# Optimization experiments

Measured on AMD Instinct MI355X. Metric: run time of the kernel, lower is better.

The kernel has to match this reference:

```python
import jax, jax.numpy as jnp
import numpy as np

NUM_HEADS = 16
HEAD_DIM = 64
HIDDEN = NUM_HEADS * HEAD_DIM  # 1024
MAX_POS = 1024


def setup_inputs() -> dict:
    key = jax.random.key(0)
    ks = jax.random.split(key, 6)
    B, L, H = 8, 1024, HIDDEN
    hidden_states = jax.random.normal(ks[0], (B, L, H), dtype=jnp.float32)
    attention_mask = jnp.zeros((B, 1, 1, L), dtype=jnp.float32)
    scale = 0.02  # keep pre-softmax logits in a sane range
    Wq = jax.random.normal(ks[1], (H, H), dtype=jnp.float32) * scale
    Wk = jax.random.normal(ks[2], (H, H), dtype=jnp.float32) * scale
    Wv = jax.random.normal(ks[3], (H, H), dtype=jnp.float32) * scale
    bq = jnp.zeros((H,), dtype=jnp.float32)
    bk = jnp.zeros((H,), dtype=jnp.float32)
    bv = jnp.zeros((H,), dtype=jnp.float32)
    dist_emb = jax.random.normal(ks[4], (2 * MAX_POS - 1, HEAD_DIM), dtype=jnp.float32) * scale
    return {"hidden_states": hidden_states, "attention_mask": attention_mask,
            "Wq": Wq, "bq": bq, "Wk": Wk, "bk": bk, "Wv": Wv, "bv": bv,
            "dist_emb": dist_emb}


def _split_heads(x):
    # [B, L, H] -> [B, nH, L, hd]
    B, L, _ = x.shape
    return x.reshape(B, L, NUM_HEADS, HEAD_DIM).transpose(0, 2, 1, 3)


def reference(hidden_states, attention_mask, Wq, bq, Wk, bk, Wv, bv, dist_emb):
    B, L, H = hidden_states.shape
    q = _split_heads(hidden_states @ Wq.T + bq)  # [B,h,L,d]
    k = _split_heads(hidden_states @ Wk.T + bk)
    v = _split_heads(hidden_states @ Wv.T + bv)

    scores = jnp.einsum("bhld,bhrd->bhlr", q, k)

    # relative_key_query positional bias
    pos_l = jnp.arange(L)[:, None]
    pos_r = jnp.arange(L)[None, :]
    dist_idx = pos_l - pos_r + MAX_POS - 1          # [L, L], in [0, 2*MAX_POS-2]
    pos_emb = dist_emb[dist_idx]                    # [L, L, d]
    scores = scores + jnp.einsum("bhld,lrd->bhlr", q, pos_emb)
    scores = scores + jnp.einsum("bhrd,lrd->bhlr", k, pos_emb)

    scores = scores / jnp.sqrt(jnp.float32(HEAD_DIM))
    scores = scores + attention_mask                # additive mask broadcast [B,1,1,L]
    probs = jax.nn.softmax(scores, axis=-1)         # dropout = identity (eval)
    ctx = jnp.einsum("bhlr,bhrd->bhld", probs, v)
    ctx = ctx.transpose(0, 2, 1, 3).reshape(B, L, H)
    return ctx
```

## Files before the change

kernel.cpp:

```cpp
#include <hip/hip_runtime.h>
#include <stdint.h>

typedef short s16x8 __attribute__((ext_vector_type(8)));
typedef float f32x4 __attribute__((ext_vector_type(4)));

#define MFMA16(a, b, c) __builtin_amdgcn_mfma_f32_16x16x32_bf16((a), (b), (c), 0, 0, 0)

__device__ __forceinline__ ushort f2b(float f) {
  union { float f; uint32_t u; } x; x.f = f;
  uint32_t r = x.u + 0x7fffu + ((x.u >> 16) & 1u);
  return (ushort)(r >> 16);
}
__device__ __forceinline__ float b2f(ushort s) {
  union { uint32_t u; float f; } x; x.u = ((uint32_t)s) << 16;
  return x.f;
}
__device__ __forceinline__ uint32_t pack2t(float a, float b) {
  return __builtin_amdgcn_perm(__float_as_uint(b), __float_as_uint(a), 0x07060302u);
}

__global__ __launch_bounds__(256) void cast_f32_bf16(const float* __restrict__ src,
                                                     ushort* __restrict__ dst, int n) {
  int i = (blockIdx.x * 256 + threadIdx.x) * 4;
  if (i + 4 <= n) {
    float4 v = *(const float4*)(src + i);
    ushort4 o; o.x = f2b(v.x); o.y = f2b(v.y); o.z = f2b(v.z); o.w = f2b(v.w);
    *(ushort4*)(dst + i) = o;
  }
}

__device__ __forceinline__ void gload16(const void* g, void* l) {
  __builtin_amdgcn_global_load_lds((const __attribute__((address_space(1))) void*)g,
                                   (__attribute__((address_space(3))) void*)l, 16, 0, 0);
}

__global__ __launch_bounds__(256) void qkv_gemm(
    const ushort* __restrict__ hb, const ushort* __restrict__ wb,
    const float* __restrict__ bq, const float* __restrict__ bk, const float* __restrict__ bv,
    ushort* __restrict__ qb, ushort* __restrict__ kb, ushort* __restrict__ vt) {
  __shared__ ushort As[128 * 32];
  __shared__ ushort Bs[128 * 32];
  const int tid = threadIdx.x;
  const int w = tid >> 6, lane = tid & 63, quad = lane >> 4, l16 = lane & 15;
  const int m0 = blockIdx.y * 128, n0 = blockIdx.x * 128;

  const int srow = w * 32 + (lane >> 2);
  const int scol = (lane & 3) * 8;
  const ushort* ga = hb + (size_t)(m0 + srow) * 1024 + scol;
  const ushort* gw = wb + (size_t)(n0 + srow) * 1024 + scol;
  ushort* lA0 = As + (w * 32) * 32;
  ushort* lA1 = As + (w * 32 + 16) * 32;
  ushort* lB0 = Bs + (w * 32) * 32;
  ushort* lB1 = Bs + (w * 32 + 16) * 32;

  f32x4 acc[4][4];
#pragma unroll
  for (int mt = 0; mt < 4; ++mt)
#pragma unroll
    for (int nt = 0; nt < 4; ++nt) acc[mt][nt] = (f32x4){0.f, 0.f, 0.f, 0.f};

  const int wm = (w >> 1) * 64, wn = (w & 1) * 64;

  for (int k0 = 0; k0 < 1024; k0 += 32) {
    gload16(ga + k0, lA0);
    gload16(ga + k0 + 16 * 1024, lA1);
    gload16(gw + k0, lB0);
    gload16(gw + k0 + 16 * 1024, lB1);
    __syncthreads();
    s16x8 af[4], bfr[4];
#pragma unroll
    for (int mt = 0; mt < 4; ++mt)
      af[mt] = *(const s16x8*)(As + (wm + 16 * mt + l16) * 32 + quad * 8);
#pragma unroll
    for (int nt = 0; nt < 4; ++nt)
      bfr[nt] = *(const s16x8*)(Bs + (wn + 16 * nt + l16) * 32 + quad * 8);
#pragma unroll
    for (int mt = 0; mt < 4; ++mt)
#pragma unroll
      for (int nt = 0; nt < 4; ++nt)
        acc[mt][nt] = MFMA16(af[mt], bfr[nt], acc[mt][nt]);
    __syncthreads();
  }

  const int mat = n0 >> 10;
  const float* bias = (mat == 0) ? bq : ((mat == 1) ? bk : bv);
  const int b = m0 >> 10;
#pragma unroll
  for (int mt = 0; mt < 4; ++mt) {
    int mbase = m0 + wm + 16 * mt + 4 * quad;
#pragma unroll
    for (int nt = 0; nt < 4; ++nt) {
      int n = n0 + wn + 16 * nt + l16;
      int o = n & 1023; int hh = o >> 6; int d = o & 63;
      float bsv = bias[o];
#pragma unroll
      for (int reg = 0; reg < 4; ++reg) {
        int l = (mbase + reg) & 1023;
        ushort bx = f2b(acc[mt][nt][reg] + bsv);
        if (mat == 0)      qb[(((size_t)(b * 16 + hh)) * 1024 + l) * 64 + d] = bx;
        else if (mat == 1) kb[(((size_t)(b * 16 + hh)) * 1024 + l) * 64 + d] = bx;
        else               vt[(((size_t)(b * 16 + hh)) * 64 + d) * 1024 + l] = bx;
      }
    }
  }
}

#define KR  0
#define VR  8192
#define ER  16384
#define SER 28672
#define PR  35072

__device__ __forceinline__ const s16x8* fragp(const ushort* base, int row, int cb) {
  return (const s16x8*)(base + row * 64 + ((cb ^ (row & 7)) * 8));
}

__global__ __launch_bounds__(256, 2) void attn_kernel(
    const ushort* __restrict__ qb, const ushort* __restrict__ kb,
    const ushort* __restrict__ vt, const ushort* __restrict__ eb,
    const float* __restrict__ mask, float* __restrict__ out) {
  __shared__ __align__(16) ushort sm[39168];
  const int tid = threadIdx.x;
  const int w = tid >> 6, lane = tid & 63, quad = lane >> 4, l16 = lane & 15;
  const int bh = blockIdx.y, b = bh >> 4, h = bh & 15;
  const int l0 = blockIdx.x * 64;

  const int srow = lane >> 3;
  const int colb = ((lane & 7) ^ srow) * 8;
  const int row0 = w * 8 + srow;

  const ushort* kp = kb + ((size_t)bh * 1024 + row0) * 64 + colb;
  const ushort* vp = vt + ((size_t)bh * 64 + row0) * 1024 + colb;
  const float* maskp = mask + b * 1024 + l16;

  const int p0 = blockIdx.x % 3;

  {
    const ushort* qp = qb + ((size_t)bh * 1024 + l0 + row0) * 64 + colb;
    gload16(qp,         sm + PR + w * 512);
    gload16(qp + 2048,  sm + PR + 2048 + w * 512);
    gload16(kp,         sm + KR + w * 512);
    gload16(kp + 2048,  sm + KR + 2048 + w * 512);
    gload16(vp,         sm + VR + w * 512);
    gload16(vp + 32768, sm + VR + 2048 + w * 512);
    const int t0i = l0 + 960;
#pragma unroll
    for (int c2 = 0; c2 < 4; ++c2) {
      int jb = w * 8 + 32 * c2;
      int seg = p0 + (jb >> 6); if (seg >= 3) seg -= 3;
      int t = t0i + jb + srow; if (t > 2046) t = 2046;
      gload16(eb + (size_t)t * 64 + colb, sm + ER + seg * 4096 + (jb & 63) * 64);
    }
  }
  __syncthreads();

  s16x8 aq0, aq1;
  {
    int r = w * 16 + l16;
    aq0 = *fragp(sm + PR, r, quad);
    aq1 = *fragp(sm + PR, r, quad + 4);
  }

  float rsum[4];
  f32x4 o_acc[4];
#pragma unroll
  for (int r = 0; r < 4; ++r) rsum[r] = 0.f;
#pragma unroll
  for (int nt = 0; nt < 4; ++nt) o_acc[nt] = (f32x4){0.f, 0.f, 0.f, 0.f};

  const float LOG2E = 1.44269504088896f;
  const float SC = 0.125f * LOG2E;

  int s0 = p0;

  for (int it = 0; it < 16; ++it) {
    const int p = it & 1;
    const int r0 = it * 64;
    if (it > 0) __syncthreads();

    {
      const int rn = (r0 + 64) & 1023;
      gload16(kp + rn * 64,        sm + KR + 4096 * (1 - p) + w * 512);
      gload16(kp + rn * 64 + 2048, sm + KR + 4096 * (1 - p) + 2048 + w * 512);
      gload16(vp + rn,             sm + VR + 4096 * (1 - p) + w * 512);
      gload16(vp + rn + 32768,     sm + VR + 4096 * (1 - p) + 2048 + w * 512);
      int pnew = s0 + 2; if (pnew >= 3) pnew -= 3;
      const int tb = l0 + 960 - r0 - 64;
#pragma unroll
      for (int c2 = 0; c2 < 2; ++c2) {
        int o = w * 8 + 32 * c2;
        int t = tb + o + srow; t = t < 0 ? 0 : (t > 2046 ? 2046 : t);
        gload16(eb + (size_t)t * 64 + colb, sm + ER + pnew * 4096 + o * 64);
      }
    }
    float mkv[4];
#pragma unroll
    for (int nt = 0; nt < 4; ++nt) mkv[nt] = maskp[r0 + 16 * nt] * LOG2E;

    const ushort* Kb = sm + KR + 4096 * p;
    const int sA = s0; int sB = s0 + 1; if (sB >= 3) sB -= 3;

    f32x4 zv[4];
#pragma unroll
    for (int nt = 0; nt < 4; ++nt) {
      int r = 16 * nt + l16;
      s16x8 bk0 = *fragp(Kb, r, quad);
      s16x8 bk1 = *fragp(Kb, r, quad + 4);
      f32x4 z = (f32x4){0.f, 0.f, 0.f, 0.f};
      z = MFMA16(aq0, bk0, z);
      z = MFMA16(aq1, bk1, z);
      zv[nt] = z;
    }
    s16x8 ak0, ak1;
    {
      int r = w * 16 + l16;
      ak0 = *fragp(Kb, r, quad);
      ak1 = *fragp(Kb, r, quad + 4);
    }

    f32x4 d1[5];
#pragma unroll
    for (int i = 0; i < 5; ++i) {
      int blk = w + i;
      int seg = (blk & 4) ? sB : sA;
      int row = seg * 64 + (blk & 3) * 16 + l16;
      s16x8 be0 = *fragp(sm + ER, row, quad);
      s16x8 be1 = *fragp(sm + ER, row, quad + 4);
      f32x4 z = (f32x4){0.f, 0.f, 0.f, 0.f};
      z = MFMA16(aq0, be0, z);
      z = MFMA16(aq1, be1, z);
      d1[i] = z;
    }
#pragma unroll
    for (int r = 0; r < 4; ++r) {
      int idx = (quad * 16 + ((4 * quad + r + 15 - l16) & 15)) * 4;
      float bp[5];
#pragma unroll
      for (int i = 0; i < 5; ++i)
        bp[i] = __int_as_float(__builtin_amdgcn_ds_bpermute(idx, __float_as_int(d1[i][r])));
      bool cnd = (4 * quad + r) > l16;
#pragma unroll
      for (int nt = 0; nt < 4; ++nt)
        zv[nt][r] += cnd ? bp[4 - nt] : bp[3 - nt];
    }

#pragma unroll
    for (int i = 0; i < 5; ++i) {
      int blk = 3 - w + i;
      int seg = (blk & 4) ? sB : sA;
      int row = seg * 64 + (blk & 3) * 16 + l16;
      s16x8 be0 = *fragp(sm + ER, row, quad);
      s16x8 be1 = *fragp(sm + ER, row, quad + 4);
      f32x4 z = (f32x4){0.f, 0.f, 0.f, 0.f};
      z = MFMA16(ak0, be0, z);
      z = MFMA16(ak1, be1, z);
      uint2 pk; pk.x = pack2t(z[0], z[1]); pk.y = pack2t(z[2], z[3]);
      *(uint2*)(sm + SER + w * 1600 + (16 * i + l16) * 20 + 4 * quad) = pk;
    }
    __syncthreads();

    const int bb = (w * 16 + 4 * quad + 15 - l16) * 20 + l16;
#pragma unroll
    for (int nt = 0; nt < 4; ++nt) {
#pragma unroll
      for (int reg = 0; reg < 4; ++reg) {
        float z2 = (zv[nt][reg] + b2f(sm[SER + bb + nt * 1600 + reg * 20])) * SC + mkv[nt];
        float pe = exp2f(z2);
        zv[nt][reg] = pe;
        rsum[reg] += pe;
      }
    }

#pragma unroll
    for (int nt = 0; nt < 4; ++nt) {
      int r = 16 * nt + l16;
      int rcb = r >> 3, rlo = r & 7;
#pragma unroll
      for (int reg = 0; reg < 4; ++reg) {
        int l = w * 16 + 4 * quad + reg;
        sm[PR + l * 64 + ((rcb ^ (l & 7)) * 8) + rlo] = f2b(zv[nt][reg]);
      }
    }
    __syncthreads();

    const ushort* Vb = sm + VR + 4096 * p;
#pragma unroll
    for (int kk = 0; kk < 2; ++kk) {
      s16x8 ap = *fragp(sm + PR, w * 16 + l16, kk * 4 + quad);
#pragma unroll
      for (int nt = 0; nt < 4; ++nt) {
        s16x8 bvf = *fragp(Vb, 16 * nt + l16, kk * 4 + quad);
        o_acc[nt] = MFMA16(ap, bvf, o_acc[nt]);
      }
    }

    s0 = (s0 == 0) ? 2 : s0 - 1;
  }

#pragma unroll
  for (int off = 1; off < 16; off <<= 1)
#pragma unroll
    for (int reg = 0; reg < 4; ++reg)
      rsum[reg] += __shfl_xor(rsum[reg], off);

#pragma unroll
  for (int nt = 0; nt < 4; ++nt)
#pragma unroll
    for (int reg = 0; reg < 4; ++reg) {
      int l = l0 + w * 16 + 4 * quad + reg;
      int d = 16 * nt + l16;
      out[((size_t)(b * 1024 + l)) * 1024 + h * 64 + d] = o_acc[nt][reg] / rsum[reg];
    }
}

extern "C" void kernel_launch(void* const* d_in, const int* in_sizes, int n_in,
                              void* d_out, int out_size, void* d_ws, size_t ws_size,
                              hipStream_t stream) {
  const float* hidden = (const float*)d_in[0];
  const float* mask   = (const float*)d_in[1];
  const float* Wq     = (const float*)d_in[2];
  const float* bq     = (const float*)d_in[3];
  const float* Wk     = (const float*)d_in[4];
  const float* bk     = (const float*)d_in[5];
  const float* Wv     = (const float*)d_in[6];
  const float* bv     = (const float*)d_in[7];
  const float* dist   = (const float*)d_in[8];
  float* out = (float*)d_out;

  ushort* ws = (ushort*)d_ws;
  ushort* qb = ws;
  ushort* kb = ws + 8388608;
  ushort* vt = ws + 16777216;
  ushort* hb = ws + 25165824;
  ushort* wb = ws + 33554432;
  ushort* eb = ws + 36700160;

  cast_f32_bf16<<<8192, 256, 0, stream>>>(hidden, hb, 8388608);
  cast_f32_bf16<<<1024, 256, 0, stream>>>(Wq, wb, 1048576);
  cast_f32_bf16<<<1024, 256, 0, stream>>>(Wk, wb + 1048576, 1048576);
  cast_f32_bf16<<<1024, 256, 0, stream>>>(Wv, wb + 2097152, 1048576);
  cast_f32_bf16<<<128, 256, 0, stream>>>(dist, eb, 131008);

  qkv_gemm<<<dim3(24, 64), 256, 0, stream>>>(hb, wb, bq, bk, bv, qb, kb, vt);
  attn_kernel<<<dim3(16, 128), 256, 0, stream>>>(qb, kb, vt, eb, mask, out);
}
```

Measured before the change: 387.2 us.

## Load K/V MFMA fragments directly from global memory and raise attention occupancy

The attention kernel no longer stages K and V tiles through double-buffered LDS. Each lane now loads its K and V MFMA operand fragments straight from global memory (relying on L2 reuse across blocks), which cuts LDS from about 78KB to 45KB and lets launch bounds request 3 blocks per CU. The QKV projection epilogue also writes the transposed V with packed 4-element stores instead of scalar ones. In exchange, K/V global loads are issued within the same iteration they are consumed, with no software prefetch, so load latency may be exposed. Each K row is also fetched redundantly by all four waves.

```diff
diff --git a/kernel.cpp b/kernel.cpp
--- a/kernel.cpp
+++ b/kernel.cpp
@@ -88,38 +88,42 @@
 #pragma unroll
   for (int mt = 0; mt < 4; ++mt) {
     int mbase = m0 + wm + 16 * mt + 4 * quad;
+    int lb = mbase & 1023;
 #pragma unroll
     for (int nt = 0; nt < 4; ++nt) {
       int n = n0 + wn + 16 * nt + l16;
       int o = n & 1023; int hh = o >> 6; int d = o & 63;
       float bsv = bias[o];
-#pragma unroll
-      for (int reg = 0; reg < 4; ++reg) {
-        int l = (mbase + reg) & 1023;
-        ushort bx = f2b(acc[mt][nt][reg] + bsv);
-        if (mat == 0)      qb[(((size_t)(b * 16 + hh)) * 1024 + l) * 64 + d] = bx;
-        else if (mat == 1) kb[(((size_t)(b * 16 + hh)) * 1024 + l) * 64 + d] = bx;
-        else               vt[(((size_t)(b * 16 + hh)) * 64 + d) * 1024 + l] = bx;
-      }
-    }
-  }
-}
-
-#define KR  0
-#define VR  8192
-#define ER  16384
-#define SER 28672
-#define PR  35072
+      if (mat == 2) {
+        ushort4 pk;
+        pk.x = f2b(acc[mt][nt][0] + bsv);
+        pk.y = f2b(acc[mt][nt][1] + bsv);
+        pk.z = f2b(acc[mt][nt][2] + bsv);
+        pk.w = f2b(acc[mt][nt][3] + bsv);
+        *(ushort4*)(vt + (((size_t)(b * 16 + hh)) * 64 + d) * 1024 + lb) = pk;
+      } else {
+        ushort* dst = (mat == 0) ? qb : kb;
+#pragma unroll
+        for (int reg = 0; reg < 4; ++reg)
+          dst[(((size_t)(b * 16 + hh)) * 1024 + lb + reg) * 64 + d] = f2b(acc[mt][nt][reg] + bsv);
+      }
+    }
+  }
+}
+
+#define ER  0
+#define SER 12288
+#define PR  18688
 
 __device__ __forceinline__ const s16x8* fragp(const ushort* base, int row, int cb) {
   return (const s16x8*)(base + row * 64 + ((cb ^ (row & 7)) * 8));
 }
 
-__global__ __launch_bounds__(256, 2) void attn_kernel(
+__global__ __launch_bounds__(256, 3) void attn_kernel(
     const ushort* __restrict__ qb, const ushort* __restrict__ kb,
     const ushort* __restrict__ vt, const ushort* __restrict__ eb,
     const float* __restrict__ mask, float* __restrict__ out) {
-  __shared__ __align__(16) ushort sm[39168];
+  __shared__ __align__(16) ushort sm[22784];
   const int tid = threadIdx.x;
   const int w = tid >> 6, lane = tid & 63, quad = lane >> 4, l16 = lane & 15;
   const int bh = blockIdx.y, b = bh >> 4, h = bh & 15;
@@ -129,8 +133,8 @@
   const int colb = ((lane & 7) ^ srow) * 8;
   const int row0 = w * 8 + srow;
 
-  const ushort* kp = kb + ((size_t)bh * 1024 + row0) * 64 + colb;
-  const ushort* vp = vt + ((size_t)bh * 64 + row0) * 1024 + colb;
+  const ushort* kgl = kb + (size_t)bh * 65536 + l16 * 64 + quad * 8;
+  const ushort* vgl = vt + (size_t)bh * 65536 + l16 * 1024 + quad * 8;
   const float* maskp = mask + b * 1024 + l16;
 
   const int p0 = blockIdx.x % 3;
@@ -139,10 +143,6 @@
     const ushort* qp = qb + ((size_t)bh * 1024 + l0 + row0) * 64 + colb;
     gload16(qp,         sm + PR + w * 512);
     gload16(qp + 2048,  sm + PR + 2048 + w * 512);
-    gload16(kp,         sm + KR + w * 512);
-    gload16(kp + 2048,  sm + KR + 2048 + w * 512);
-    gload16(vp,         sm + VR + w * 512);
-    gload16(vp + 32768, sm + VR + 2048 + w * 512);
     const int t0i = l0 + 960;
 #pragma unroll
     for (int c2 = 0; c2 < 4; ++c2) {
@@ -174,16 +174,10 @@
   int s0 = p0;
 
   for (int it = 0; it < 16; ++it) {
-    const int p = it & 1;
     const int r0 = it * 64;
     if (it > 0) __syncthreads();
 
     {
-      const int rn = (r0 + 64) & 1023;
-      gload16(kp + rn * 64,        sm + KR + 4096 * (1 - p) + w * 512);
-      gload16(kp + rn * 64 + 2048, sm + KR + 4096 * (1 - p) + 2048 + w * 512);
-      gload16(vp + rn,             sm + VR + 4096 * (1 - p) + w * 512);
-      gload16(vp + rn + 32768,     sm + VR + 4096 * (1 - p) + 2048 + w * 512);
       int pnew = s0 + 2; if (pnew >= 3) pnew -= 3;
       const int tb = l0 + 960 - r0 - 64;
 #pragma unroll
@@ -193,29 +187,37 @@
         gload16(eb + (size_t)t * 64 + colb, sm + ER + pnew * 4096 + o * 64);
       }
     }
+
+    s16x8 bkf[4][2], akf[2], bvf[4][2];
+    {
+      const ushort* kit = kgl + r0 * 64;
+#pragma unroll
+      for (int nt = 0; nt < 4; ++nt) {
+        bkf[nt][0] = *(const s16x8*)(kit + nt * 1024);
+        bkf[nt][1] = *(const s16x8*)(kit + nt * 1024 + 32);
+      }
+      akf[0] = *(const s16x8*)(kit + w * 1024);
+      akf[1] = *(const s16x8*)(kit + w * 1024 + 32);
+      const ushort* vit = vgl + r0;
+#pragma unroll
+      for (int nt = 0; nt < 4; ++nt) {
+        bvf[nt][0] = *(const s16x8*)(vit + nt * 16384);
+        bvf[nt][1] = *(const s16x8*)(vit + nt * 16384 + 32);
+      }
+    }
     float mkv[4];
 #pragma unroll
     for (int nt = 0; nt < 4; ++nt) mkv[nt] = maskp[r0 + 16 * nt] * LOG2E;
 
-    const ushort* Kb = sm + KR + 4096 * p;
     const int sA = s0; int sB = s0 + 1; if (sB >= 3) sB -= 3;
 
     f32x4 zv[4];
 #pragma unroll
     for (int nt = 0; nt < 4; ++nt) {
-      int r = 16 * nt + l16;
-      s16x8 bk0 = *fragp(Kb, r, quad);
-      s16x8 bk1 = *fragp(Kb, r, quad + 4);
       f32x4 z = (f32x4){0.f, 0.f, 0.f, 0.f};
-      z = MFMA16(aq0, bk0, z);
-      z = MFMA16(aq1, bk1, z);
+      z = MFMA16(aq0, bkf[nt][0], z);
+      z = MFMA16(aq1, bkf[nt][1], z);
       zv[nt] = z;
-    }
-    s16x8 ak0, ak1;
-    {
-      int r = w * 16 + l16;
-      ak0 = *fragp(Kb, r, quad);
-      ak1 = *fragp(Kb, r, quad + 4);
     }
 
     f32x4 d1[5];
@@ -252,8 +254,8 @@
       s16x8 be0 = *fragp(sm + ER, row, quad);
       s16x8 be1 = *fragp(sm + ER, row, quad + 4);
       f32x4 z = (f32x4){0.f, 0.f, 0.f, 0.f};
-      z = MFMA16(ak0, be0, z);
-      z = MFMA16(ak1, be1, z);
+      z = MFMA16(akf[0], be0, z);
+      z = MFMA16(akf[1], be1, z);
       uint2 pk; pk.x = pack2t(z[0], z[1]); pk.y = pack2t(z[2], z[3]);
       *(uint2*)(sm + SER + w * 1600 + (16 * i + l16) * 20 + 4 * quad) = pk;
     }
@@ -283,15 +285,12 @@
     }
     __syncthreads();
 
-    const ushort* Vb = sm + VR + 4096 * p;
 #pragma unroll
     for (int kk = 0; kk < 2; ++kk) {
       s16x8 ap = *fragp(sm + PR, w * 16 + l16, kk * 4 + quad);
 #pragma unroll
-      for (int nt = 0; nt < 4; ++nt) {
-        s16x8 bvf = *fragp(Vb, 16 * nt + l16, kk * 4 + quad);
-        o_acc[nt] = MFMA16(ap, bvf, o_acc[nt]);
-      }
+      for (int nt = 0; nt < 4; ++nt)
+        o_acc[nt] = MFMA16(ap, bvf[nt][kk], o_acc[nt]);
     }
 
     s0 = (s0 == 0) ? 2 : s0 - 1;
```

Result: slower. 460.4 us (+18.9%).
